# Kernel optimization log

Hardware: AMD Instinct MI355X
Metric: run time of the kernel (lower is better)

## Reference

```python
import jax, jax.numpy as jnp
import numpy as np

B, T, M, D, H, DH = 2, 2048, 2048, 384, 4, 96
NM, DF, R, NA = 8, 1536, 16, 4
S = 0.02  # weight init scale

PARAM_NAMES = ['cWq','cbq','cWk','cbk','cWv','cbv','cWo','cbo',
               'sWq','sbq','sWk','sbk','sWv','sbv','sWo','sbo',
               'gW','gb','f1W','f1b','f2W','f2b','adA','adB',
               'ln1g','ln1b','ln2g','ln2b','ln3g','ln3b']

def setup_inputs() -> dict:
    key = jax.random.key(0)
    ks = jax.random.split(key, 20)
    n = lambda k, sh, s=1.0: jax.random.normal(k, sh, dtype=jnp.float32) * s
    z = lambda sh: jnp.zeros(sh, dtype=jnp.float32)
    o = lambda sh: jnp.ones(sh, dtype=jnp.float32)
    return {
        'x': n(ks[0], (B, T, D)),
        'mem': n(ks[1], (B, M, D)),
        'motif_ctrl': n(ks[2], (B, NM)),
        'adapter_idx': 1,
        'cWq': n(ks[3], (D, D), S), 'cbq': z((D,)),
        'cWk': n(ks[4], (D, D), S), 'cbk': z((D,)),
        'cWv': n(ks[5], (D, D), S), 'cbv': z((D,)),
        'cWo': n(ks[6], (D, D), S), 'cbo': z((D,)),
        'sWq': n(ks[7], (D, D), S), 'sbq': z((D,)),
        'sWk': n(ks[8], (D, D), S), 'sbk': z((D,)),
        'sWv': n(ks[9], (D, D), S), 'sbv': z((D,)),
        'sWo': n(ks[10], (D, D), S), 'sbo': z((D,)),
        'gW': n(ks[11], (H, NM), S), 'gb': z((H,)),
        'f1W': n(ks[12], (DF, D), S), 'f1b': z((DF,)),
        'f2W': n(ks[13], (D, DF), S), 'f2b': z((D,)),
        'adA': n(ks[14], (NA, R, D), S),
        'adB': n(ks[15], (NA, D, R), S),
        'ln1g': o((D,)), 'ln1b': z((D,)),
        'ln2g': o((D,)), 'ln2b': z((D,)),
        'ln3g': o((D,)), 'ln3b': z((D,)),
    }

def _lin(x, W, b):
    return x @ W.T + b  # torch nn.Linear convention: W is [out, in]

def _layernorm(x, g, b):
    mu = x.mean(-1, keepdims=True)
    var = ((x - mu) ** 2).mean(-1, keepdims=True)
    return (x - mu) * jax.lax.rsqrt(var + 1e-5) * g + b

def _block(x, mem, motif_ctrl, adapter_idx, p):
    scale = 1.0 / np.sqrt(DH).astype(np.float32)
    # --- cross-attention over memory ---
    h = _layernorm(x, p['ln1g'], p['ln1b'])
    q = _lin(h, p['cWq'], p['cbq']).reshape(B, T, H, DH)
    k = _lin(mem, p['cWk'], p['cbk']).reshape(B, M, H, DH)
    v = _lin(mem, p['cWv'], p['cbv']).reshape(B, M, H, DH)
    A = jax.nn.softmax(jnp.einsum('bthd,bmhd->bhtm', q, k) * scale, axis=-1)
    z = jnp.einsum('bhtm,bmhd->bthd', A, v).reshape(B, T, D)
    x = x + _lin(z, p['cWo'], p['cbo'])
    # --- motif-gated self-attention (post-softmax per-head gate) ---
    h = _layernorm(x, p['ln2g'], p['ln2b'])
    gates = jax.nn.sigmoid(motif_ctrl @ p['gW'].T + p['gb'])  # [B, H]
    q = _lin(h, p['sWq'], p['sbq']).reshape(B, T, H, DH)
    k = _lin(h, p['sWk'], p['sbk']).reshape(B, T, H, DH)
    v = _lin(h, p['sWv'], p['sbv']).reshape(B, T, H, DH)
    A = jax.nn.softmax(jnp.einsum('bthd,bshd->bhts', q, k) * scale, axis=-1)
    A = A * gates[:, :, None, None]
    z = jnp.einsum('bhts,bshd->bthd', A, v).reshape(B, T, D)
    x = x + _lin(z, p['sWo'], p['sbo'])
    # --- LoRA-adapter FFN ---
    h = _layernorm(x, p['ln3g'], p['ln3b'])
    f = _lin(jax.nn.gelu(_lin(h, p['f1W'], p['f1b']), approximate=False), p['f2W'], p['f2b'])
    f = f + (h @ p['adA'][adapter_idx].T) @ p['adB'][adapter_idx].T
    return x + f

def reference(x, mem, motif_ctrl, adapter_idx,
              cWq, cbq, cWk, cbk, cWv, cbv, cWo, cbo,
              sWq, sbq, sWk, sbk, sWv, sbv, sWo, sbo,
              gW, gb, f1W, f1b, f2W, f2b, adA, adB,
              ln1g, ln1b, ln2g, ln2b, ln3g, ln3b):
    p = dict(zip(PARAM_NAMES, (cWq, cbq, cWk, cbk, cWv, cbv, cWo, cbo,
                               sWq, sbq, sWk, sbk, sWv, sbv, sWo, sbo,
                               gW, gb, f1W, f1b, f2W, f2b, adA, adB,
                               ln1g, ln1b, ln2g, ln2b, ln3g, ln3b)))
    return _block(x, mem, motif_ctrl, int(adapter_idx), p)
```

## Files before the change

kernel.cpp:

```cpp
#include <hip/hip_runtime.h>
#include <hip/hip_bf16.h>
#include <math.h>

#define B_   2
#define T_   2048
#define M_   2048
#define D_   384
#define H_   4
#define DH_  96
#define NM_  8
#define DF_  1536
#define R_   16
#define NR_  4096
#define SPL  8

typedef unsigned short u16;
typedef u16    u16x8  __attribute__((ext_vector_type(8)));
typedef u16    u16x4  __attribute__((ext_vector_type(4)));
typedef __bf16 bf16x8 __attribute__((ext_vector_type(8)));
typedef float  f32x4  __attribute__((ext_vector_type(4)));

union V8 { u16x8 u; bf16x8 b; };
__device__ __forceinline__ bf16x8 as_bf(u16x8 x) { V8 v; v.u = x; return v.b; }

__device__ __forceinline__ u16 f2bf(float f) {
    unsigned u = __float_as_uint(f);
    unsigned r = (u + 0x7fffu + ((u >> 16) & 1u)) >> 16;
    return (u16)r;
}
__device__ __forceinline__ float bf2f(u16 u) {
    return __uint_as_float(((unsigned)u) << 16);
}

__device__ __forceinline__ void load16(const u16* g, u16* l) {
    __builtin_amdgcn_global_load_lds(
        (const __attribute__((address_space(1))) void*)g,
        (__attribute__((address_space(3))) void*)l, 16, 0, 0);
}

__global__ __launch_bounds__(256)
void setup_kernel(const float* cWq, const float* cWk, const float* cWv, const float* cWo,
                  const float* sWq, const float* sWk, const float* sWv, const float* sWo,
                  const float* f1W, const float* f2W, const float* adA, const float* adB,
                  const float* mem,
                  u16* Wqkv_c, u16* Wco, u16* Wqkv_s, u16* Wso,
                  u16* Wf1, u16* Wf2, u16* WadA, u16* WadB, u16* memb,
                  const float* cbq, const float* cbk, const float* cbv,
                  const float* sbq, const float* sbk, const float* sbv,
                  float* bqkv_c, float* bqkv_s,
                  const float* mc, const float* gW, const float* gb, float* gates) {
    int seg = blockIdx.y;
    if (seg == 13) {
        for (int i = blockIdx.x * 256 + threadIdx.x; i < 2312; i += gridDim.x * 256) {
            if (i < 1152) {
                bqkv_c[i] = (i < 384) ? cbq[i] : (i < 768 ? cbk[i - 384] : cbv[i - 768]);
            } else if (i < 2304) {
                int j = i - 1152;
                bqkv_s[j] = (j < 384) ? sbq[j] : (j < 768 ? sbk[j - 384] : sbv[j - 768]);
            } else {
                int k = i - 2304;
                int b = k / H_, h = k % H_;
                float s = gb[h];
                for (int n = 0; n < NM_; n++)
                    s += mc[b * NM_ + n] * gW[h * NM_ + n];
                gates[k] = 1.f / (1.f + __expf(-s));
            }
        }
        return;
    }
    const float* s; u16* d; int n;
    switch (seg) {
        case 0:  s = cWq; d = Wqkv_c;           n = 147456; break;
        case 1:  s = cWk; d = Wqkv_c + 147456;  n = 147456; break;
        case 2:  s = cWv; d = Wqkv_c + 294912;  n = 147456; break;
        case 3:  s = cWo; d = Wco;              n = 147456; break;
        case 4:  s = sWq; d = Wqkv_s;           n = 147456; break;
        case 5:  s = sWk; d = Wqkv_s + 147456;  n = 147456; break;
        case 6:  s = sWv; d = Wqkv_s + 294912;  n = 147456; break;
        case 7:  s = sWo; d = Wso;              n = 147456; break;
        case 8:  s = f1W; d = Wf1;              n = 589824; break;
        case 9:  s = f2W; d = Wf2;              n = 589824; break;
        case 10: s = adA; d = WadA;             n = 24576;  break;
        case 11: s = adB; d = WadB;             n = 24576;  break;
        default: s = mem; d = memb;             n = 1572864; break;
    }
    for (int i = blockIdx.x * 256 + threadIdx.x; i < n; i += gridDim.x * 256)
        d[i] = f2bf(s[i]);
}

__global__ __launch_bounds__(384)
void ln_kernel(const float* __restrict__ x, const float* __restrict__ g,
               const float* __restrict__ b, u16* __restrict__ out) {
    __shared__ float sm[8];
    int row = blockIdx.x;
    int t = threadIdx.x;
    float v = x[(long)row * D_ + t];

    float s = v;
    for (int o = 32; o > 0; o >>= 1) s += __shfl_down(s, o);
    if ((t & 63) == 0) sm[t >> 6] = s;
    __syncthreads();
    float mu = 0.f;
    for (int i = 0; i < 6; i++) mu += sm[i];
    mu *= (1.f / D_);
    __syncthreads();

    float d = v - mu;
    s = d * d;
    for (int o = 32; o > 0; o >>= 1) s += __shfl_down(s, o);
    if ((t & 63) == 0) sm[t >> 6] = s;
    __syncthreads();
    float var = 0.f;
    for (int i = 0; i < 6; i++) var += sm[i];
    var *= (1.f / D_);

    float r = rsqrtf(var + 1e-5f);
    out[(long)row * D_ + t] = f2bf(d * r * g[t] + b[t]);
}

template<int MT, int ACT, bool OBF, bool VT, bool LORA, bool LORAA>
__global__ __launch_bounds__(256)
void gemm_uni(const u16* __restrict__ A0, const u16* __restrict__ A1, int aswitch,
              const u16* __restrict__ W, const float* __restrict__ bias,
              const float* __restrict__ res, void* __restrict__ Cout, int NC, int K,
              u16* __restrict__ Vt, int vtbase,
              const u16* __restrict__ Tl, const u16* __restrict__ adW,
              u16* __restrict__ TlOut, const int* __restrict__ aidx) {
    constexpr int NREG = 4 * MT + 8;
    constexpr int HALF = NREG * 512;
    __shared__ __align__(16) u16 S[2 * HALF];
    int tid = threadIdx.x, w = tid >> 6, lane = tid & 63;
    int l15 = lane & 15, quad = lane >> 4;
    int bm = blockIdx.y * (MT * 32), bn = blockIdx.x * 64;
    bool loraBlk = LORAA && (bn >= NC);

    const u16* Ap = (bn < aswitch) ? A0 : A1;
    const u16* Wb = W;
    if (LORAA && loraBlk) Wb = adW + (long)aidx[0] * 6144;

    const u16* GP[MT + 2];
    int LO[MT + 2];
    #pragma unroll
    for (int i = 0; i < MT + 2; i++) {
        int r = i * 4 + w;
        const u16* src;
        if (r < 4 * MT) {
            int mt = r >> 1, kc = r & 1;
            src = Ap + (long)(bm + mt * 16 + l15) * K + kc * 32 + quad * 8;
        } else {
            int rw = r - 4 * MT, nt = rw >> 1, kc = rw & 1;
            if (LORAA && loraBlk)
                src = Wb + (long)((nt * 16 + l15) & 15) * K + kc * 32 + quad * 8;
            else
                src = Wb + (long)(bn + nt * 16 + l15) * K + kc * 32 + quad * 8;
        }
        GP[i] = src;
        LO[i] = r * 512;
    }

    f32x4 acc[MT][2];
    #pragma unroll
    for (int s = 0; s < MT; s++)
        #pragma unroll
        for (int j = 0; j < 2; j++) acc[s][j] = (f32x4){0.f, 0.f, 0.f, 0.f};

    int niter = K >> 6;
    #pragma unroll
    for (int i = 0; i < MT + 2; i++) load16(GP[i], S + LO[i]);

    for (int it = 0; it < niter; it++) {
        __syncthreads();
        int cur = (it & 1) * HALF, nxt = HALF - cur;
        if (it + 1 < niter) {
            int k = (it + 1) << 6;
            #pragma unroll
            for (int i = 0; i < MT + 2; i++) load16(GP[i] + k, S + nxt + LO[i]);
        }
        #pragma unroll
        for (int kc = 0; kc < 2; kc++) {
            u16x8 af[MT], bfv[2];
            #pragma unroll
            for (int s = 0; s < MT; s++)
                af[s] = *(const u16x8*)(S + cur + (((w & 1) * MT + s) * 2 + kc) * 512 + lane * 8);
            #pragma unroll
            for (int j = 0; j < 2; j++)
                bfv[j] = *(const u16x8*)(S + cur + (4 * MT + (((w >> 1) * 2 + j) * 2 + kc)) * 512 + lane * 8);
            #pragma unroll
            for (int s = 0; s < MT; s++)
                #pragma unroll
                for (int j = 0; j < 2; j++)
                    acc[s][j] = __builtin_amdgcn_mfma_f32_16x16x32_bf16(
                        as_bf(af[s]), as_bf(bfv[j]), acc[s][j], 0, 0, 0);
        }
    }

    if (LORA) {
        long ao = (long)aidx[0] * 6144;
        u16x8 tlf[MT], adf[2];
        #pragma unroll
        for (int s = 0; s < MT; s++) {
            #pragma unroll
            for (int e = 0; e < 8; e++) tlf[s][e] = 0;
            if (quad < 2)
                tlf[s] = *(const u16x8*)(Tl + (long)(bm + ((w & 1) * MT + s) * 16 + l15) * 16 + quad * 8);
        }
        #pragma unroll
        for (int j = 0; j < 2; j++) {
            #pragma unroll
            for (int e = 0; e < 8; e++) adf[j][e] = 0;
            if (quad < 2)
                adf[j] = *(const u16x8*)(adW + ao + (long)(bn + ((w >> 1) * 2 + j) * 16 + l15) * 16 + quad * 8);
        }
        #pragma unroll
        for (int s = 0; s < MT; s++)
            #pragma unroll
            for (int j = 0; j < 2; j++)
                acc[s][j] = __builtin_amdgcn_mfma_f32_16x16x32_bf16(
                    as_bf(tlf[s]), as_bf(adf[j]), acc[s][j], 0, 0, 0);
    }

    #pragma unroll
    for (int mi = 0; mi < MT; mi++) {
        int mt = (w & 1) * MT + mi;
        int rowb = bm + mt * 16 + quad * 4;
        #pragma unroll
        for (int nj = 0; nj < 2; nj++) {
            int coll = ((w >> 1) * 2 + nj) * 16 + l15;
            int col = bn + coll;
            if (LORAA && loraBlk) {
                if (coll < 16) {
                    #pragma unroll
                    for (int r = 0; r < 4; r++)
                        TlOut[(long)(rowb + r) * 16 + coll] = f2bf(acc[mi][nj][r]);
                }
            } else {
                float bv = bias ? bias[col] : 0.f;
                if (VT && col >= vtbase) {
                    int vc = col - vtbase;
                    int b = rowb >> 11, rowl = rowb & 2047;
                    u16x4 ov;
                    #pragma unroll
                    for (int r = 0; r < 4; r++) ov[r] = f2bf(acc[mi][nj][r] + bv);
                    *(u16x4*)(Vt + ((long)b * 384 + vc) * 2048 + rowl) = ov;
                } else {
                    #pragma unroll
                    for (int r = 0; r < 4; r++) {
                        float v = acc[mi][nj][r] + bv;
                        if (ACT == 1) v = 0.5f * v * (1.f + erff(v * 0.70710678118654752f));
                        long idx = (long)(rowb + r) * NC + col;
                        if (res) v += res[idx];
                        if (OBF) ((u16*)Cout)[idx] = f2bf(v);
                        else     ((float*)Cout)[idx] = v;
                    }
                }
            }
        }
    }
}

__global__ __launch_bounds__(256)
void attn_mfma(const u16* __restrict__ Qg, int qs,
               const u16* __restrict__ Kg, int ks,
               const u16* __restrict__ Vt,
               u16* __restrict__ Po, float* __restrict__ Pl) {
    __shared__ __align__(16) u16 Ks[2][6144];
    __shared__ __align__(16) u16 Vs[6144];
    __shared__ __align__(16) u16 Ps[4][2][1024];
    const float SCALE = 0.10206207261596575f;

    int tid = threadIdx.x, wv = tid >> 6, lane = tid & 63;
    int l15 = lane & 15, quad = lane >> 4;
    int bh = blockIdx.y, b = bh >> 2, h = bh & 3;
    int split = blockIdx.z;
    int q0 = blockIdx.x * 128 + wv * 32;

    const u16* Qb = Qg + (long)(b * 2048 + q0) * qs + h * 96;
    const u16* Kb = Kg + (long)(b * 2048 + split * 256) * ks + h * 96;
    const u16* Vb = Vt + (long)(b * 384 + h * 96) * 2048 + split * 256;

    u16x8 qf[2][3];
    #pragma unroll
    for (int g = 0; g < 2; g++)
        #pragma unroll
        for (int t = 0; t < 3; t++)
            qf[g][t] = *(const u16x8*)(Qb + (long)(g * 16 + l15) * qs + t * 32 + quad * 8);

    f32x4 o[2][6];
    #pragma unroll
    for (int g = 0; g < 2; g++)
        #pragma unroll
        for (int i = 0; i < 6; i++) o[g][i] = (f32x4){0.f, 0.f, 0.f, 0.f};
    float rs[2][4] = {{0.f, 0.f, 0.f, 0.f}, {0.f, 0.f, 0.f, 0.f}};

    const u16* KgI[3]; int KlO[3]; const u16* VgI[3]; u16* VlP[3];
    #pragma unroll
    for (int i = 0; i < 3; i++) {
        int r = i * 4 + wv;
        int ksub = r & 3, kst = r >> 2;
        KgI[i] = Kb + (long)(ksub * 16 + l15) * ks + kst * 32 + quad * 8;
        KlO[i] = (ksub * 3 + kst) * 512;
        int nt = r >> 1, t2 = r & 1;
        VgI[i] = Vb + (long)(nt * 16 + l15) * 2048 + t2 * 32 + quad * 8;
        VlP[i] = &Vs[0] + r * 512;
    }

    #pragma unroll
    for (int i = 0; i < 3; i++) load16(KgI[i], &Ks[0][0] + KlO[i]);

    for (int it = 0; it < 4; it++) {
        int cur = it & 1, nxt = cur ^ 1;
        __syncthreads();
        int j = it * 64;
        #pragma unroll
        for (int i = 0; i < 3; i++) load16(VgI[i] + j, VlP[i]);
        if (it + 1 < 4) {
            int jn = (it + 1) * 64;
            #pragma unroll
            for (int i = 0; i < 3; i++) load16(KgI[i] + (long)jn * ks, &Ks[nxt][0] + KlO[i]);
        }

        f32x4 sc[2][4];
        #pragma unroll
        for (int g = 0; g < 2; g++)
            #pragma unroll
            for (int s = 0; s < 4; s++) sc[g][s] = (f32x4){0.f, 0.f, 0.f, 0.f};
        #pragma unroll
        for (int s = 0; s < 4; s++)
            #pragma unroll
            for (int t = 0; t < 3; t++) {
                u16x8 kf = *(const u16x8*)(&Ks[cur][0] + (s * 3 + t) * 512 + lane * 8);
                sc[0][s] = __builtin_amdgcn_mfma_f32_16x16x32_bf16(as_bf(qf[0][t]), as_bf(kf), sc[0][s], 0, 0, 0);
                sc[1][s] = __builtin_amdgcn_mfma_f32_16x16x32_bf16(as_bf(qf[1][t]), as_bf(kf), sc[1][s], 0, 0, 0);
            }

        #pragma unroll
        for (int g = 0; g < 2; g++)
            #pragma unroll
            for (int s = 0; s < 4; s++) {
                int base = (s >> 1) * 512 + ((((s & 1) << 1) | (l15 >> 3))) * 128 + (l15 & 7);
                #pragma unroll
                for (int r = 0; r < 4; r++) {
                    float p = __expf(sc[g][s][r] * SCALE);
                    rs[g][r] += p;
                    Ps[wv][g][base + (quad * 4 + r) * 8] = f2bf(p);
                }
            }

        __syncthreads();
        #pragma unroll
        for (int t2 = 0; t2 < 2; t2++) {
            u16x8 pf0 = *(const u16x8*)(&Ps[wv][0][0] + t2 * 512 + quad * 128 + l15 * 8);
            u16x8 pf1 = *(const u16x8*)(&Ps[wv][1][0] + t2 * 512 + quad * 128 + l15 * 8);
            #pragma unroll
            for (int nt = 0; nt < 6; nt++) {
                u16x8 vf = *(const u16x8*)(&Vs[0] + (nt * 2 + t2) * 512 + lane * 8);
                o[0][nt] = __builtin_amdgcn_mfma_f32_16x16x32_bf16(as_bf(pf0), as_bf(vf), o[0][nt], 0, 0, 0);
                o[1][nt] = __builtin_amdgcn_mfma_f32_16x16x32_bf16(as_bf(pf1), as_bf(vf), o[1][nt], 0, 0, 0);
            }
        }
    }

    #pragma unroll
    for (int off = 1; off < 16; off <<= 1)
        #pragma unroll
        for (int g = 0; g < 2; g++)
            #pragma unroll
            for (int r = 0; r < 4; r++) rs[g][r] += __shfl_xor(rs[g][r], off);

    #pragma unroll
    for (int g = 0; g < 2; g++) {
        u16* Pob = Po + ((long)(split * 8 + bh) * 2048 + q0 + g * 16) * 96;
        #pragma unroll
        for (int nt = 0; nt < 6; nt++)
            #pragma unroll
            for (int r = 0; r < 4; r++)
                Pob[(long)(quad * 4 + r) * 96 + nt * 16 + l15] = f2bf(o[g][nt][r]);
        if (l15 == 0) {
            long mb = (long)(split * 8 + bh) * 2048 + q0 + g * 16 + quad * 4;
            #pragma unroll
            for (int r = 0; r < 4; r++) Pl[mb + r] = rs[g][r];
        }
    }
}

__global__ __launch_bounds__(256)
void attn_combine(const u16* __restrict__ Po, const float* __restrict__ Pl,
                  const float* __restrict__ gates, u16* __restrict__ Z) {
    int bh = blockIdx.y, b = bh >> 2, h = bh & 3;
    int tid = threadIdx.x;
    int rl = tid >> 2, part = tid & 3;
    int row = blockIdx.x * 64 + rl;
    long rbase = (long)bh * 2048 + row;

    float L = 0.f;
    #pragma unroll
    for (int s = 0; s < SPL; s++) L += Pl[s * 16384 + rbase];
    float g = gates ? gates[bh] : 1.f;
    float sc = g / L;

    u16* Zr = Z + ((long)(b * 2048) + row) * 384 + h * 96 + part * 24;
    #pragma unroll
    for (int i = 0; i < 24; i += 4) {
        f32x4 acc = (f32x4){0.f, 0.f, 0.f, 0.f};
        #pragma unroll
        for (int s = 0; s < SPL; s++) {
            u16x4 v = *(const u16x4*)(Po + ((long)s * 16384 + rbase) * 96 + part * 24 + i);
            #pragma unroll
            for (int e = 0; e < 4; e++) acc[e] += bf2f(v[e]);
        }
        u16x4 ov;
        #pragma unroll
        for (int e = 0; e < 4; e++) ov[e] = f2bf(acc[e] * sc);
        *(u16x4*)(Zr + i) = ov;
    }
}

extern "C" void kernel_launch(void* const* d_in, const int* in_sizes, int n_in,
                              void* d_out, int out_size, void* d_ws, size_t ws_size,
                              hipStream_t stream) {
    const float* x    = (const float*)d_in[0];
    const float* mem  = (const float*)d_in[1];
    const float* mc   = (const float*)d_in[2];
    const int*   aidx = (const int*)d_in[3];
    const float* cWq = (const float*)d_in[4],  *cbq = (const float*)d_in[5];
    const float* cWk = (const float*)d_in[6],  *cbk = (const float*)d_in[7];
    const float* cWv = (const float*)d_in[8],  *cbv = (const float*)d_in[9];
    const float* cWo = (const float*)d_in[10], *cbo = (const float*)d_in[11];
    const float* sWq = (const float*)d_in[12], *sbq = (const float*)d_in[13];
    const float* sWk = (const float*)d_in[14], *sbk = (const float*)d_in[15];
    const float* sWv = (const float*)d_in[16], *sbv = (const float*)d_in[17];
    const float* sWo = (const float*)d_in[18], *sbo = (const float*)d_in[19];
    const float* gW  = (const float*)d_in[20], *gb  = (const float*)d_in[21];
    const float* f1W = (const float*)d_in[22], *f1b = (const float*)d_in[23];
    const float* f2W = (const float*)d_in[24], *f2b = (const float*)d_in[25];
    const float* adA = (const float*)d_in[26], *adB = (const float*)d_in[27];
    const float* ln1g = (const float*)d_in[28], *ln1b = (const float*)d_in[29];
    const float* ln2g = (const float*)d_in[30], *ln2b = (const float*)d_in[31];
    const float* ln3g = (const float*)d_in[32], *ln3b = (const float*)d_in[33];

    u16* p = (u16*)d_ws;
    u16* H      = p; p += (size_t)NR_ * 384;
    u16* bufQKV = p; p += (size_t)NR_ * 1152;
    u16* Vt     = p; p += (size_t)B_ * 384 * 2048;
    u16* Zb     = p; p += (size_t)NR_ * 384;
    u16* F      = p; p += (size_t)NR_ * 1536;
    u16* Tl     = p; p += (size_t)NR_ * 16;
    u16* memb   = p; p += (size_t)NR_ * 384;
    u16* Wqkv_c = p; p += 442368;
    u16* Wco    = p; p += 147456;
    u16* Wqkv_s = p; p += 442368;
    u16* Wso    = p; p += 147456;
    u16* Wf1    = p; p += 589824;
    u16* Wf2    = p; p += 589824;
    u16* WadA   = p; p += 24576;
    u16* WadB   = p; p += 24576;
    u16* Po     = p; p += (size_t)SPL * 8 * 2048 * 96;
    float* fp = (float*)(((size_t)p + 3) & ~(size_t)3);
    float* X1 = fp;     fp += (size_t)NR_ * 384;
    float* X2 = fp;     fp += (size_t)NR_ * 384;
    float* Pl = fp;     fp += (size_t)SPL * 8 * 2048;
    float* bqkv_c = fp; fp += 1152;
    float* bqkv_s = fp; fp += 1152;
    float* gbuf   = fp; fp += 8;

    setup_kernel<<<dim3(96, 14), 256, 0, stream>>>(
        cWq, cWk, cWv, cWo, sWq, sWk, sWv, sWo, f1W, f2W, adA, adB, mem,
        Wqkv_c, Wco, Wqkv_s, Wso, Wf1, Wf2, WadA, WadB, memb,
        cbq, cbk, cbv, sbq, sbk, sbv, bqkv_c, bqkv_s, mc, gW, gb, gbuf);

    const float* nf = nullptr;
    const u16* nu = nullptr;
    ln_kernel<<<NR_, 384, 0, stream>>>(x, ln1g, ln1b, H);
    gemm_uni<2, 0, true, true, false, false><<<dim3(18, 64), 256, 0, stream>>>(
        H, memb, 384, Wqkv_c, bqkv_c, nf, bufQKV, 1152, 384, Vt, 768, nu, nu, nullptr, nullptr);
    attn_mfma<<<dim3(16, 8, SPL), 256, 0, stream>>>(bufQKV, 1152, bufQKV + 384, 1152, Vt, Po, Pl);
    attn_combine<<<dim3(32, 8), 256, 0, stream>>>(Po, Pl, nullptr, Zb);
    gemm_uni<1, 0, false, false, false, false><<<dim3(6, 128), 256, 0, stream>>>(
        Zb, Zb, 0, Wco, cbo, x, X1, 384, 384, nullptr, 0, nu, nu, nullptr, nullptr);

    ln_kernel<<<NR_, 384, 0, stream>>>(X1, ln2g, ln2b, H);
    gemm_uni<2, 0, true, true, false, false><<<dim3(18, 64), 256, 0, stream>>>(
        H, H, 0, Wqkv_s, bqkv_s, nf, bufQKV, 1152, 384, Vt, 768, nu, nu, nullptr, nullptr);
    attn_mfma<<<dim3(16, 8, SPL), 256, 0, stream>>>(bufQKV, 1152, bufQKV + 384, 1152, Vt, Po, Pl);
    attn_combine<<<dim3(32, 8), 256, 0, stream>>>(Po, Pl, gbuf, Zb);
    gemm_uni<1, 0, false, false, false, false><<<dim3(6, 128), 256, 0, stream>>>(
        Zb, Zb, 0, Wso, sbo, X1, X2, 384, 384, nullptr, 0, nu, nu, nullptr, nullptr);

    ln_kernel<<<NR_, 384, 0, stream>>>(X2, ln3g, ln3b, H);
    gemm_uni<2, 1, true, false, false, true><<<dim3(25, 64), 256, 0, stream>>>(
        H, H, 0, Wf1, f1b, nf, F, 1536, 384, nullptr, 0, nu, WadA, Tl, aidx);
    gemm_uni<1, 0, false, false, true, false><<<dim3(6, 128), 256, 0, stream>>>(
        F, F, 0, Wf2, f2b, X2, d_out, 384, 1536, nullptr, 0, Tl, WadB, nullptr, aidx);
}
```

Measured before the change: 363.4 us.

## Widen attention tile to 64 queries per wave with 32-key double-buffered K/V chunks

```diff
diff --git a/kernel.cpp b/kernel.cpp
--- a/kernel.cpp
+++ b/kernel.cpp
@@ -263,81 +263,89 @@
                const u16* __restrict__ Kg, int ks,
                const u16* __restrict__ Vt,
                u16* __restrict__ Po, float* __restrict__ Pl) {
-    __shared__ __align__(16) u16 Ks[2][6144];
-    __shared__ __align__(16) u16 Vs[6144];
-    __shared__ __align__(16) u16 Ps[4][2][1024];
+    __shared__ __align__(16) u16 Ks[2][3072];
+    __shared__ __align__(16) u16 Vs[2][3072];
+    __shared__ __align__(16) u16 Ps[4][4][512];
     const float SCALE = 0.10206207261596575f;
 
     int tid = threadIdx.x, wv = tid >> 6, lane = tid & 63;
     int l15 = lane & 15, quad = lane >> 4;
     int bh = blockIdx.y, b = bh >> 2, h = bh & 3;
     int split = blockIdx.z;
-    int q0 = blockIdx.x * 128 + wv * 32;
+    int q0 = blockIdx.x * 256 + wv * 64;
 
     const u16* Qb = Qg + (long)(b * 2048 + q0) * qs + h * 96;
     const u16* Kb = Kg + (long)(b * 2048 + split * 256) * ks + h * 96;
     const u16* Vb = Vt + (long)(b * 384 + h * 96) * 2048 + split * 256;
 
-    u16x8 qf[2][3];
-    #pragma unroll
-    for (int g = 0; g < 2; g++)
+    u16x8 qf[4][3];
+    #pragma unroll
+    for (int g = 0; g < 4; g++)
         #pragma unroll
         for (int t = 0; t < 3; t++)
             qf[g][t] = *(const u16x8*)(Qb + (long)(g * 16 + l15) * qs + t * 32 + quad * 8);
 
-    f32x4 o[2][6];
-    #pragma unroll
-    for (int g = 0; g < 2; g++)
+    f32x4 o[4][6];
+    #pragma unroll
+    for (int g = 0; g < 4; g++)
         #pragma unroll
         for (int i = 0; i < 6; i++) o[g][i] = (f32x4){0.f, 0.f, 0.f, 0.f};
-    float rs[2][4] = {{0.f, 0.f, 0.f, 0.f}, {0.f, 0.f, 0.f, 0.f}};
-
-    const u16* KgI[3]; int KlO[3]; const u16* VgI[3]; u16* VlP[3];
+    float rs[4][4];
+    #pragma unroll
+    for (int g = 0; g < 4; g++)
+        #pragma unroll
+        for (int r = 0; r < 4; r++) rs[g][r] = 0.f;
+
+    const u16* GI[3]; u16* LB[3]; long ST[3];
     #pragma unroll
     for (int i = 0; i < 3; i++) {
         int r = i * 4 + wv;
-        int ksub = r & 3, kst = r >> 2;
-        KgI[i] = Kb + (long)(ksub * 16 + l15) * ks + kst * 32 + quad * 8;
-        KlO[i] = (ksub * 3 + kst) * 512;
-        int nt = r >> 1, t2 = r & 1;
-        VgI[i] = Vb + (long)(nt * 16 + l15) * 2048 + t2 * 32 + quad * 8;
-        VlP[i] = &Vs[0] + r * 512;
-    }
-
-    #pragma unroll
-    for (int i = 0; i < 3; i++) load16(KgI[i], &Ks[0][0] + KlO[i]);
-
-    for (int it = 0; it < 4; it++) {
+        if (r < 6) {
+            int ksub = r / 3, kst = r - ksub * 3;
+            GI[i] = Kb + (long)(ksub * 16 + l15) * ks + kst * 32 + quad * 8;
+            LB[i] = &Ks[0][0] + r * 512;
+            ST[i] = (long)32 * ks;
+        } else {
+            int nt = r - 6;
+            GI[i] = Vb + (long)(nt * 16 + l15) * 2048 + quad * 8;
+            LB[i] = &Vs[0][0] + nt * 512;
+            ST[i] = 32;
+        }
+    }
+
+    #pragma unroll
+    for (int i = 0; i < 3; i++) load16(GI[i], LB[i]);
+
+    for (int it = 0; it < 8; it++) {
+        __syncthreads();
         int cur = it & 1, nxt = cur ^ 1;
-        __syncthreads();
-        int j = it * 64;
-        #pragma unroll
-        for (int i = 0; i < 3; i++) load16(VgI[i] + j, VlP[i]);
-        if (it + 1 < 4) {
-            int jn = (it + 1) * 64;
-            #pragma unroll
-            for (int i = 0; i < 3; i++) load16(KgI[i] + (long)jn * ks, &Ks[nxt][0] + KlO[i]);
-        }
-
-        f32x4 sc[2][4];
-        #pragma unroll
-        for (int g = 0; g < 2; g++)
-            #pragma unroll
-            for (int s = 0; s < 4; s++) sc[g][s] = (f32x4){0.f, 0.f, 0.f, 0.f};
-        #pragma unroll
-        for (int s = 0; s < 4; s++)
+        if (it + 1 < 8) {
+            #pragma unroll
+            for (int i = 0; i < 3; i++)
+                load16(GI[i] + (long)(it + 1) * ST[i], LB[i] + nxt * 3072);
+        }
+
+        f32x4 sc[4][2];
+        #pragma unroll
+        for (int g = 0; g < 4; g++)
+            #pragma unroll
+            for (int s = 0; s < 2; s++) sc[g][s] = (f32x4){0.f, 0.f, 0.f, 0.f};
+        #pragma unroll
+        for (int s = 0; s < 2; s++)
             #pragma unroll
             for (int t = 0; t < 3; t++) {
                 u16x8 kf = *(const u16x8*)(&Ks[cur][0] + (s * 3 + t) * 512 + lane * 8);
-                sc[0][s] = __builtin_amdgcn_mfma_f32_16x16x32_bf16(as_bf(qf[0][t]), as_bf(kf), sc[0][s], 0, 0, 0);
-                sc[1][s] = __builtin_amdgcn_mfma_f32_16x16x32_bf16(as_bf(qf[1][t]), as_bf(kf), sc[1][s], 0, 0, 0);
+                #pragma unroll
+                for (int g = 0; g < 4; g++)
+                    sc[g][s] = __builtin_amdgcn_mfma_f32_16x16x32_bf16(
+                        as_bf(qf[g][t]), as_bf(kf), sc[g][s], 0, 0, 0);
             }
 
         #pragma unroll
-        for (int g = 0; g < 2; g++)
-            #pragma unroll
-            for (int s = 0; s < 4; s++) {
-                int base = (s >> 1) * 512 + ((((s & 1) << 1) | (l15 >> 3))) * 128 + (l15 & 7);
+        for (int g = 0; g < 4; g++)
+            #pragma unroll
+            for (int s = 0; s < 2; s++) {
+                int base = (((s << 1) | (l15 >> 3))) * 128 + (l15 & 7);
                 #pragma unroll
                 for (int r = 0; r < 4; r++) {
                     float p = __expf(sc[g][s][r] * SCALE);
@@ -346,29 +354,29 @@
                 }
             }
 
-        __syncthreads();
-        #pragma unroll
-        for (int t2 = 0; t2 < 2; t2++) {
-            u16x8 pf0 = *(const u16x8*)(&Ps[wv][0][0] + t2 * 512 + quad * 128 + l15 * 8);
-            u16x8 pf1 = *(const u16x8*)(&Ps[wv][1][0] + t2 * 512 + quad * 128 + l15 * 8);
-            #pragma unroll
-            for (int nt = 0; nt < 6; nt++) {
-                u16x8 vf = *(const u16x8*)(&Vs[0] + (nt * 2 + t2) * 512 + lane * 8);
-                o[0][nt] = __builtin_amdgcn_mfma_f32_16x16x32_bf16(as_bf(pf0), as_bf(vf), o[0][nt], 0, 0, 0);
-                o[1][nt] = __builtin_amdgcn_mfma_f32_16x16x32_bf16(as_bf(pf1), as_bf(vf), o[1][nt], 0, 0, 0);
-            }
+        u16x8 pf[4];
+        #pragma unroll
+        for (int g = 0; g < 4; g++)
+            pf[g] = *(const u16x8*)(&Ps[wv][g][0] + quad * 128 + l15 * 8);
+        #pragma unroll
+        for (int nt = 0; nt < 6; nt++) {
+            u16x8 vf = *(const u16x8*)(&Vs[cur][0] + nt * 512 + lane * 8);
+            #pragma unroll
+            for (int g = 0; g < 4; g++)
+                o[g][nt] = __builtin_amdgcn_mfma_f32_16x16x32_bf16(
+                    as_bf(pf[g]), as_bf(vf), o[g][nt], 0, 0, 0);
         }
     }
 
     #pragma unroll
     for (int off = 1; off < 16; off <<= 1)
         #pragma unroll
-        for (int g = 0; g < 2; g++)
+        for (int g = 0; g < 4; g++)
             #pragma unroll
             for (int r = 0; r < 4; r++) rs[g][r] += __shfl_xor(rs[g][r], off);
 
     #pragma unroll
-    for (int g = 0; g < 2; g++) {
+    for (int g = 0; g < 4; g++) {
         u16* Pob = Po + ((long)(split * 8 + bh) * 2048 + q0 + g * 16) * 96;
         #pragma unroll
         for (int nt = 0; nt < 6; nt++)
@@ -473,7 +481,7 @@
     ln_kernel<<<NR_, 384, 0, stream>>>(x, ln1g, ln1b, H);
     gemm_uni<2, 0, true, true, false, false><<<dim3(18, 64), 256, 0, stream>>>(
         H, memb, 384, Wqkv_c, bqkv_c, nf, bufQKV, 1152, 384, Vt, 768, nu, nu, nullptr, nullptr);
-    attn_mfma<<<dim3(16, 8, SPL), 256, 0, stream>>>(bufQKV, 1152, bufQKV + 384, 1152, Vt, Po, Pl);
+    attn_mfma<<<dim3(8, 8, SPL), 256, 0, stream>>>(bufQKV, 1152, bufQKV + 384, 1152, Vt, Po, Pl);
     attn_combine<<<dim3(32, 8), 256, 0, stream>>>(Po, Pl, nullptr, Zb);
     gemm_uni<1, 0, false, false, false, false><<<dim3(6, 128), 256, 0, stream>>>(
         Zb, Zb, 0, Wco, cbo, x, X1, 384, 384, nullptr, 0, nu, nu, nullptr, nullptr);
@@ -481,7 +489,7 @@
     ln_kernel<<<NR_, 384, 0, stream>>>(X1, ln2g, ln2b, H);
     gemm_uni<2, 0, true, true, false, false><<<dim3(18, 64), 256, 0, stream>>>(
         H, H, 0, Wqkv_s, bqkv_s, nf, bufQKV, 1152, 384, Vt, 768, nu, nu, nullptr, nullptr);
-    attn_mfma<<<dim3(16, 8, SPL), 256, 0, stream>>>(bufQKV, 1152, bufQKV + 384, 1152, Vt, Po, Pl);
+    attn_mfma<<<dim3(8, 8, SPL), 256, 0, stream>>>(bufQKV, 1152, bufQKV + 384, 1152, Vt, Po, Pl);
     attn_combine<<<dim3(32, 8), 256, 0, stream>>>(Po, Pl, gbuf, Zb);
     gemm_uni<1, 0, false, false, false, false><<<dim3(6, 128), 256, 0, stream>>>(
         Zb, Zb, 0, Wso, sbo, X1, X2, 384, 384, nullptr, 0, nu, nu, nullptr, nullptr);
```

Result: no change. 365.1 us (+0.5%).
